# Optimization experiments

Hardware: AMD Instinct MI355X
Metric: run time of the kernel (lower is better)

The kernel has to match this reference:

```python
import jax, jax.numpy as jnp
import numpy as np

EPS = 1e-13

def masked_softmax(scores, mask):
    # scores: [B, L1, L2], mask: [B, L2] binary float
    # ESIM-style: softmax(scores * mask) * mask, renormalized.
    m = mask[:, None, :]                      # [B, 1, L2]
    r = jax.nn.softmax(scores * m, axis=-1) * m
    return r / (r.sum(axis=-1, keepdims=True) + EPS)

def weighted_sum(attn, tensor, mask):
    # attn: [B, L1, L2], tensor: [B, L2, D], mask: [B, L1]
    return jnp.matmul(attn, tensor) * mask[:, :, None]

def setup_inputs() -> dict:
    key = jax.random.key(0)
    k1, k2, k3, k4 = jax.random.split(key, 4)
    B, Lp, Lh, D = 64, 512, 512, 600
    encoded_premise = jax.random.normal(k1, (B, Lp, D), dtype=jnp.float32)
    encoded_hypothesis = jax.random.normal(k2, (B, Lh, D), dtype=jnp.float32)
    # binary padding masks (1 = valid token)
    premise_mask = (jax.random.uniform(k3, (B, Lp)) > 0.15).astype(jnp.float32)
    hypothesis_mask = (jax.random.uniform(k4, (B, Lh)) > 0.15).astype(jnp.float32)
    return {"encoded_premise": encoded_premise, "premise_mask": premise_mask,
            "encoded_hypothesis": encoded_hypothesis, "hypothesis_mask": hypothesis_mask}

def reference(encoded_premise, premise_mask, encoded_hypothesis, hypothesis_mask):
    # shared cross-attention score matrix [B, Lp, Lh]
    attn = jnp.einsum('bpd,bhd->bph', encoded_premise, encoded_hypothesis)
    a_p = masked_softmax(attn, hypothesis_mask)                    # [B, Lp, Lh]
    a_h = masked_softmax(attn.transpose(0, 2, 1), premise_mask)    # [B, Lh, Lp]
    weighted_premise = weighted_sum(a_p, encoded_hypothesis, premise_mask)      # [B, Lp, D]
    weighted_hypothesis = weighted_sum(a_h, encoded_premise, hypothesis_mask)   # [B, Lh, D]
    return (weighted_premise, weighted_hypothesis)
```

## Files before the change

kernel.cpp:

```cpp
#include <hip/hip_runtime.h>
#include <hip/hip_bf16.h>

#define DEVB 64
#define LSEQ 512
#define DDIM 600

typedef short short8 __attribute__((ext_vector_type(8)));
typedef float f32x4 __attribute__((ext_vector_type(4)));
typedef _Float16 f16x8 __attribute__((ext_vector_type(8)));
typedef _Float16 f16x4 __attribute__((ext_vector_type(4)));

constexpr int LDP = 40;

__device__ __forceinline__ unsigned short f2bf(float x) {
    union { float f; unsigned u; } v; v.f = x;
    unsigned r = v.u + 0x7fffu + ((v.u >> 16) & 1u);
    return (unsigned short)(r >> 16);
}
__device__ __forceinline__ f32x4 mfma16(short8 a, short8 b, f32x4 c) {
    return __builtin_amdgcn_mfma_f32_16x16x32_bf16(a, b, c, 0, 0, 0);
}
__device__ __forceinline__ f32x4 mfma16h(f16x8 a, f16x8 b, f32x4 c) {
    return __builtin_amdgcn_mfma_f32_16x16x32_f16(a, b, c, 0, 0, 0);
}

__global__ __launch_bounds__(256) void prep_both(
    const float* __restrict__ P, const float* __restrict__ H,
    _Float16* __restrict__ Phi, _Float16* __restrict__ Plo,
    _Float16* __restrict__ Hhi,
    _Float16* __restrict__ pT, _Float16* __restrict__ hT)
{
    int blk = blockIdx.x;
    const float* X; _Float16 *Xhi, *Xlo, *XT;
    if (blk < DEVB * 80) { X = P; Xhi = Phi; Xlo = Plo; XT = pT; }
    else { blk -= DEVB * 80; X = H; Xhi = Hhi; Xlo = nullptr; XT = hT; }

    int b   = blk / 80;
    int rem = blk % 80;
    int r0  = (rem / 10) << 6;
    int d0  = (rem % 10) << 6;
    const float* Xb = X + (size_t)b * LSEQ * DDIM;
    _Float16* Hib = Xhi + (size_t)b * LSEQ * DDIM;
    _Float16* Lob = Xlo ? (Xlo + (size_t)b * LSEQ * DDIM) : nullptr;

    __shared__ _Float16 T[64 * 66];
    int t = threadIdx.x;
#pragma unroll
    for (int it = 0; it < 2; ++it) {
        int g  = t + (it << 8);
        int ri = g >> 3;
        int dc = (g & 7) << 3;
        if (d0 + dc < DDIM) {
            const float* src = Xb + (size_t)(r0 + ri) * DDIM + d0 + dc;
            float4 x0 = *(const float4*)src;
            float4 x1 = *(const float4*)(src + 4);
            f16x8 hi, lo;
            hi[0] = (_Float16)x0.x; lo[0] = (_Float16)(x0.x - (float)hi[0]);
            hi[1] = (_Float16)x0.y; lo[1] = (_Float16)(x0.y - (float)hi[1]);
            hi[2] = (_Float16)x0.z; lo[2] = (_Float16)(x0.z - (float)hi[2]);
            hi[3] = (_Float16)x0.w; lo[3] = (_Float16)(x0.w - (float)hi[3]);
            hi[4] = (_Float16)x1.x; lo[4] = (_Float16)(x1.x - (float)hi[4]);
            hi[5] = (_Float16)x1.y; lo[5] = (_Float16)(x1.y - (float)hi[5]);
            hi[6] = (_Float16)x1.z; lo[6] = (_Float16)(x1.z - (float)hi[6]);
            hi[7] = (_Float16)x1.w; lo[7] = (_Float16)(x1.w - (float)hi[7]);
            *(f16x8*)(Hib + (size_t)(r0 + ri) * DDIM + d0 + dc) = hi;
            if (Lob) *(f16x8*)(Lob + (size_t)(r0 + ri) * DDIM + d0 + dc) = lo;
#pragma unroll
            for (int j = 0; j < 8; ++j)
                T[(dc + j) * 66 + ri] = hi[j];
        }
    }
    if (XT) {
        __syncthreads();
        int d  = t >> 2;
        int ch = (t & 3) << 4;
        if (d0 + d < DDIM) {
            unsigned buf[8];
#pragma unroll
            for (int i = 0; i < 8; ++i)
                buf[i] = *(const unsigned*)&T[d * 66 + ch + 2 * i];
            unsigned* dst = (unsigned*)(XT + ((size_t)b * DDIM + d0 + d) * LSEQ + r0 + ch);
            *(uint4*)(dst)     = *(uint4*)&buf[0];
            *(uint4*)(dst + 4) = *(uint4*)&buf[4];
        }
    }
}

__global__ __launch_bounds__(256) void attn_gemm(
    const _Float16* __restrict__ Phi, const _Float16* __restrict__ Plo,
    const _Float16* __restrict__ Hhi, float* __restrict__ attn)
{
    const int bid = blockIdx.x;
    const int swz = (bid & 7) * 128 + (bid >> 3);
    const int b  = swz >> 4;
    const int pt = ((swz >> 2) & 3) << 7;
    const int ht = (swz & 3) << 7;
    const _Float16* Pbh = Phi + ((size_t)b * LSEQ + pt) * DDIM;
    const _Float16* Pbl = Plo + ((size_t)b * LSEQ + pt) * DDIM;
    const _Float16* Hb  = Hhi + ((size_t)b * LSEQ + ht) * DDIM;
    float* Ab = attn + (size_t)b * LSEQ * LSEQ;

    __shared__ _Float16 Ah[2][128 * 32], Al[2][128 * 32], Bh[2][128 * 32];

    const int t    = threadIdx.x;
    const int lane = t & 63;
    const int wave = t >> 6;
    const int wm = (wave >> 1) << 6;
    const int wn = (wave & 1) << 6;
    const int fr = lane & 15;
    const int fq = lane >> 4;
    const int srow = t >> 2;
    const int sc8  = (t & 3) << 3;

    const int wchunk = (t & 3) ^ ((srow >> 1) & 3);
    const int woff   = srow * 32 + (wchunk << 3);
    const int rcoff  = ((fq ^ ((fr >> 1) & 3)) << 3);

    f16x8 pf[6];
    const f16x8 zz = {0, 0, 0, 0, 0, 0, 0, 0};
    auto issue = [&](int k0) {
        bool ok = (k0 + sc8) < DDIM;
#pragma unroll
        for (int r = 0; r < 2; ++r) {
            size_t off = (size_t)(srow + (r << 6)) * DDIM + k0 + sc8;
            pf[r * 3 + 0] = ok ? *(const f16x8*)(Pbh + off) : zz;
            pf[r * 3 + 1] = ok ? *(const f16x8*)(Pbl + off) : zz;
            pf[r * 3 + 2] = ok ? *(const f16x8*)(Hb  + off) : zz;
        }
    };
    auto wr = [&](int buf) {
#pragma unroll
        for (int r = 0; r < 2; ++r) {
            int off = woff + (r << 11);
            *(f16x8*)&Ah[buf][off] = pf[r * 3 + 0];
            *(f16x8*)&Al[buf][off] = pf[r * 3 + 1];
            *(f16x8*)&Bh[buf][off] = pf[r * 3 + 2];
        }
    };

    issue(0);
    wr(0);
    issue(32);
    __syncthreads();

    f32x4 acc[4][4];
#pragma unroll
    for (int i = 0; i < 4; ++i)
#pragma unroll
        for (int j = 0; j < 4; ++j) acc[i][j] = (f32x4){0.f, 0.f, 0.f, 0.f};

    constexpr int NK = 19;
    int cur = 0;
    for (int it = 0; it < NK; ++it) {
        f16x8 ah[4], al[4], bh[4];
#pragma unroll
        for (int i = 0; i < 4; ++i) {
            int ra = (wm + (i << 4) + fr) * 32 + rcoff;
            int rb = (wn + (i << 4) + fr) * 32 + rcoff;
            ah[i] = *(const f16x8*)&Ah[cur][ra];
            al[i] = *(const f16x8*)&Al[cur][ra];
            bh[i] = *(const f16x8*)&Bh[cur][rb];
        }
        if (it + 1 < NK) {
            wr(cur ^ 1);
            if (it + 2 < NK) issue((it + 2) << 5);
        }
#pragma unroll
        for (int mi = 0; mi < 4; ++mi)
#pragma unroll
            for (int ni = 0; ni < 4; ++ni) {
                f32x4 c = acc[mi][ni];
                c = mfma16h(ah[mi], bh[ni], c);
                c = mfma16h(al[mi], bh[ni], c);
                acc[mi][ni] = c;
            }
        __syncthreads();
        cur ^= 1;
    }

#pragma unroll
    for (int mi = 0; mi < 4; ++mi)
#pragma unroll
        for (int ni = 0; ni < 4; ++ni)
#pragma unroll
            for (int j = 0; j < 4; ++j) {
                int p = pt + wm + (mi << 4) + (fq << 2) + j;
                int h = ht + wn + (ni << 4) + fr;
                Ab[(size_t)p * LSEQ + h] = acc[mi][ni][j];
            }
}

__global__ __launch_bounds__(256) void stats_w1(
    const float* __restrict__ attn, const float* __restrict__ hmask,
    const float* __restrict__ pmask,
    float* __restrict__ M1, float* __restrict__ R1,
    _Float16* __restrict__ W1,
    float* __restrict__ Mp, float* __restrict__ Tp, float* __restrict__ Sp)
{
    int b      = blockIdx.x >> 3;
    int stripe = blockIdx.x & 7;
    int lane   = threadIdx.x & 63;
    int wave   = threadIdx.x >> 6;
    const float* hm = hmask + (b << 9);
    const float* pm = pmask + (b << 9);

    float4 m0 = *(const float4*)(hm + (lane << 3));
    float4 m1 = *(const float4*)(hm + (lane << 3) + 4);
    float mk[8] = {m0.x, m0.y, m0.z, m0.w, m1.x, m1.y, m1.z, m1.w};

    float cM[8], cT[8], cS[8];
#pragma unroll
    for (int j = 0; j < 8; ++j) { cM[j] = -1e30f; cT[j] = 0.f; cS[j] = 0.f; }

    for (int i = 0; i < 16; ++i) {
        int row   = (stripe << 6) + (wave << 4) + i;
        int rowid = (b << 9) + row;
        const float* rp = attn + (size_t)rowid * LSEQ + (lane << 3);
        float4 s0 = *(const float4*)rp;
        float4 s1 = *(const float4*)(rp + 4);
        float s[8] = {s0.x, s0.y, s0.z, s0.w, s1.x, s1.y, s1.z, s1.w};

        float v[8];
#pragma unroll
        for (int j = 0; j < 8; ++j) v[j] = s[j] * mk[j];
        float mx = -1e30f;
#pragma unroll
        for (int j = 0; j < 8; ++j) mx = fmaxf(mx, v[j]);
#pragma unroll
        for (int off = 32; off; off >>= 1) mx = fmaxf(mx, __shfl_xor(mx, off));

        float e[8], T = 0.f, S = 0.f;
#pragma unroll
        for (int j = 0; j < 8; ++j) { e[j] = __expf(v[j] - mx); T += mk[j] * e[j]; S += e[j]; }
#pragma unroll
        for (int off = 32; off; off >>= 1) { T += __shfl_xor(T, off); S += __shfl_xor(S, off); }
        float R = 1.f / (T + 1e-13f * S);

        if (W1) {
            union { f16x8 v8; _Float16 h[8]; } wv;
#pragma unroll
            for (int j = 0; j < 8; ++j) wv.h[j] = (_Float16)(mk[j] * e[j] * R);
            *(f16x8*)(W1 + (size_t)rowid * LSEQ + (lane << 3)) = wv.v8;
        }
        if (lane == 0) { M1[rowid] = mx; R1[rowid] = R; }

        float pmv = pm[row];
#pragma unroll
        for (int j = 0; j < 8; ++j) {
            float v2 = s[j] * pmv;
            float nm = fmaxf(cM[j], v2);
            float sc = __expf(cM[j] - nm);
            float e2 = __expf(v2 - nm);
            cT[j] = cT[j] * sc + pmv * e2;
            cS[j] = cS[j] * sc + e2;
            cM[j] = nm;
        }
    }

    __shared__ float LM[4][512], LT[4][512], LS[4][512];
#pragma unroll
    for (int j = 0; j < 8; ++j) {
        int c = (lane << 3) + j;
        LM[wave][c] = cM[j]; LT[wave][c] = cT[j]; LS[wave][c] = cS[j];
    }
    __syncthreads();

    size_t base = (size_t)((b << 3) + stripe) * 512;
    for (int cc = threadIdx.x; cc < 512; cc += 256) {
        float gm = fmaxf(fmaxf(LM[0][cc], LM[1][cc]), fmaxf(LM[2][cc], LM[3][cc]));
        float gT = 0.f, gS = 0.f;
#pragma unroll
        for (int w = 0; w < 4; ++w) {
            float sc = __expf(LM[w][cc] - gm);
            gT += LT[w][cc] * sc;
            gS += LS[w][cc] * sc;
        }
        Mp[base + cc] = gm; Tp[base + cc] = gT; Sp[base + cc] = gS;
    }
}

__global__ __launch_bounds__(256) void col_merge(
    const float* __restrict__ Mp, const float* __restrict__ Tp,
    const float* __restrict__ Sp, float* __restrict__ M2, float* __restrict__ R2)
{
    int b = blockIdx.x >> 1;
    int c = ((blockIdx.x & 1) << 8) + threadIdx.x;
    float gm = -1e30f, gT = 0.f, gS = 0.f;
#pragma unroll
    for (int st = 0; st < 8; ++st) {
        size_t idx = (size_t)((b << 3) + st) * 512 + c;
        float m = Mp[idx], tt = Tp[idx], ss = Sp[idx];
        float nm  = fmaxf(gm, m);
        float sc1 = __expf(gm - nm), sc2 = __expf(m - nm);
        gT = gT * sc1 + tt * sc2;
        gS = gS * sc1 + ss * sc2;
        gm = nm;
    }
    M2[(b << 9) + c] = gm;
    R2[(b << 9) + c] = 1.f / (gT + 1e-13f * gS);
}

__global__ __launch_bounds__(256) void w2gen_m(
    const float* __restrict__ attn, const float* __restrict__ pmask,
    const float* __restrict__ Mp, const float* __restrict__ Tp,
    const float* __restrict__ Sp, _Float16* __restrict__ W2)
{
    int blk = blockIdx.x;
    int b  = blk >> 5;
    int p0 = ((blk >> 2) & 7) << 6;
    int h0 = (blk & 3) << 7;
    const float* Ab = attn + (size_t)b * LSEQ * LSEQ;
    const float* pm = pmask + (b << 9);

    __shared__ float sM[128], sR[128];
    __shared__ _Float16 T[128 * 66];
    int t = threadIdx.x;
    if (t < 128) {
        float gm = -1e30f, gT = 0.f, gS = 0.f;
#pragma unroll
        for (int st = 0; st < 8; ++st) {
            size_t idx = (size_t)((b << 3) + st) * 512 + h0 + t;
            float m = Mp[idx], tt = Tp[idx], ss = Sp[idx];
            float nm  = fmaxf(gm, m);
            float sc1 = __expf(gm - nm), sc2 = __expf(m - nm);
            gT = gT * sc1 + tt * sc2;
            gS = gS * sc1 + ss * sc2;
            gm = nm;
        }
        sM[t] = gm;
        sR[t] = 1.f / (gT + 1e-13f * gS);
    }
    __syncthreads();

#pragma unroll
    for (int it = 0; it < 8; ++it) {
        int g  = t + (it << 8);
        int pi = g >> 5;
        int hc = (g & 31) << 2;
        float4 x = *(const float4*)(Ab + (size_t)(p0 + pi) * LSEQ + h0 + hc);
        float pv = pm[p0 + pi];
        _Float16 w0 = 0, w1 = 0, w2 = 0, w3 = 0;
        if (pv != 0.f) {
            w0 = (_Float16)(__expf(x.x - sM[hc + 0]) * sR[hc + 0]);
            w1 = (_Float16)(__expf(x.y - sM[hc + 1]) * sR[hc + 1]);
            w2 = (_Float16)(__expf(x.z - sM[hc + 2]) * sR[hc + 2]);
            w3 = (_Float16)(__expf(x.w - sM[hc + 3]) * sR[hc + 3]);
        }
        T[(hc + 0) * 66 + pi] = w0;
        T[(hc + 1) * 66 + pi] = w1;
        T[(hc + 2) * 66 + pi] = w2;
        T[(hc + 3) * 66 + pi] = w3;
    }
    __syncthreads();

    int h  = t >> 1;
    int po = (t & 1) << 5;
    unsigned buf[16];
#pragma unroll
    for (int i = 0; i < 16; ++i)
        buf[i] = *(const unsigned*)&T[h * 66 + po + 2 * i];
    unsigned* dst = (unsigned*)(W2 + ((size_t)(b << 9) + h0 + h) * LSEQ + p0 + po);
#pragma unroll
    for (int i = 0; i < 4; ++i)
        *(uint4*)(dst + 4 * i) = *(uint4*)&buf[4 * i];
}

__global__ __launch_bounds__(256) void gemm_fp16(
    const _Float16* __restrict__ W, const _Float16* __restrict__ BT,
    const float* __restrict__ mask_m, float* __restrict__ out)
{
    const int bid = blockIdx.x;
    const int swz = (bid & 7) * 160 + (bid >> 3);
    const int b   = swz / 20;
    const int rem = swz % 20;
    const int m0  = (rem / 5) << 7;
    const int n0  = (rem % 5) << 7;
    const _Float16* Wb = W  + (size_t)b * LSEQ * LSEQ;
    const _Float16* Bb = BT + (size_t)b * DDIM * LSEQ;

    __shared__ _Float16 Wl[2][128 * 32];
    __shared__ _Float16 Bl[2][128 * 32];

    const int t    = threadIdx.x;
    const int lane = t & 63;
    const int wave = t >> 6;
    const int wm = (wave >> 1) << 6;
    const int wn = (wave & 1) << 6;
    const int fr = lane & 15;
    const int fq = lane >> 4;
    const int srow = t >> 2;
    const int sc8  = (t & 3) << 3;

    const int wchunk = (t & 3) ^ ((srow >> 1) & 3);
    const int woff   = srow * 32 + (wchunk << 3);
    const int rcoff  = ((fq ^ ((fr >> 1) & 3)) << 3);

    f16x8 pw[2], pb[2];
    const f16x8 zz = {0, 0, 0, 0, 0, 0, 0, 0};
    auto issue = [&](int k0) {
#pragma unroll
        for (int r = 0; r < 2; ++r) {
            int row = srow + (r << 6);
            pw[r] = *(const f16x8*)(Wb + (size_t)(m0 + row) * LSEQ + k0 + sc8);
            int nrow = n0 + row;
            pb[r] = (nrow < DDIM) ? *(const f16x8*)(Bb + (size_t)nrow * LSEQ + k0 + sc8) : zz;
        }
    };
    auto wr = [&](int buf) {
#pragma unroll
        for (int r = 0; r < 2; ++r) {
            int off = woff + (r << 11);
            *(f16x8*)&Wl[buf][off] = pw[r];
            *(f16x8*)&Bl[buf][off] = pb[r];
        }
    };

    issue(0);
    wr(0);
    issue(32);
    __syncthreads();

    f32x4 acc[4][4];
#pragma unroll
    for (int i = 0; i < 4; ++i)
#pragma unroll
        for (int j = 0; j < 4; ++j) acc[i][j] = (f32x4){0.f, 0.f, 0.f, 0.f};

    constexpr int NK = 16;
    int cur = 0;
    for (int it = 0; it < NK; ++it) {
        f16x8 af[4], bfr[4];
#pragma unroll
        for (int i = 0; i < 4; ++i) {
            af[i]  = *(const f16x8*)&Wl[cur][(wm + (i << 4) + fr) * 32 + rcoff];
            bfr[i] = *(const f16x8*)&Bl[cur][(wn + (i << 4) + fr) * 32 + rcoff];
        }
        if (it + 1 < NK) {
            wr(cur ^ 1);
            if (it + 2 < NK) issue((it + 2) << 5);
        }
#pragma unroll
        for (int mi = 0; mi < 4; ++mi)
#pragma unroll
            for (int ni = 0; ni < 4; ++ni)
                acc[mi][ni] = mfma16h(af[mi], bfr[ni], acc[mi][ni]);
        __syncthreads();
        cur ^= 1;
    }

    const float* mmb = mask_m + (b << 9) + m0;
#pragma unroll
    for (int mi = 0; mi < 4; ++mi)
#pragma unroll
        for (int j = 0; j < 4; ++j) {
            int row = wm + (mi << 4) + (fq << 2) + j;
            float mm = mmb[row];
#pragma unroll
            for (int ni = 0; ni < 4; ++ni) {
                int d = n0 + wn + (ni << 4) + fr;
                if (d < DDIM)
                    out[((size_t)(b << 9) + m0 + row) * DDIM + d] = mm * acc[mi][ni][j];
            }
        }
}

template <int TRANSA>
__global__ __launch_bounds__(256) void wsum(
    const float* __restrict__ attn, const float* __restrict__ Bsrc,
    const float* __restrict__ mask_k, const float* __restrict__ mask_m,
    const float* __restrict__ Mst, const float* __restrict__ Rst,
    float* __restrict__ out)
{
    const int blk = blockIdx.x;
    const int b   = blk / 20;
    const int rem = blk % 20;
    const int m0  = (rem / 5) << 7;
    const int n0  = (rem % 5) << 7;

    const float* Ab  = attn + (size_t)b * LSEQ * LSEQ;
    const float* Bb  = Bsrc + (size_t)b * LSEQ * DDIM;
    const float* mkb = mask_k + (b << 9);

    __shared__ unsigned short Wl[128 * LDP];
    __shared__ unsigned short Bl[128 * LDP];
    __shared__ float Ml[128], Rl[128], Mm[128];

    const int t    = threadIdx.x;
    const int lane = t & 63;
    const int wave = t >> 6;
    const int wm = (wave >> 1) << 6;
    const int wn = (wave & 1) << 6;
    const int fr = lane & 15;
    const int fq = lane >> 4;

    if (t < 128) {
        Ml[t] = Mst[(b << 9) + m0 + t];
        Rl[t] = Rst[(b << 9) + m0 + t];
        Mm[t] = mask_m[(b << 9) + m0 + t];
    }
    __syncthreads();

    f32x4 acc[4][4];
#pragma unroll
    for (int i = 0; i < 4; ++i)
#pragma unroll
        for (int j = 0; j < 4; ++j) acc[i][j] = (f32x4){0.f, 0.f, 0.f, 0.f};

    for (int k0 = 0; k0 < LSEQ; k0 += 32) {
        if constexpr (TRANSA == 0) {
#pragma unroll
            for (int r = 0; r < 4; ++r) {
                int idx = t + (r << 8);
                int row = idx >> 3;
                int c4  = (idx & 7) << 2;
                float4 x  = *(const float4*)(Ab + (size_t)(m0 + row) * LSEQ + k0 + c4);
                float4 km = *(const float4*)(mkb + k0 + c4);
                float Mv = Ml[row], Rv = Rl[row];
                ushort4 w;
                w.x = (km.x != 0.f) ? f2bf(__expf(x.x - Mv) * Rv) : (unsigned short)0;
                w.y = (km.y != 0.f) ? f2bf(__expf(x.y - Mv) * Rv) : (unsigned short)0;
                w.z = (km.z != 0.f) ? f2bf(__expf(x.z - Mv) * Rv) : (unsigned short)0;
                w.w = (km.w != 0.f) ? f2bf(__expf(x.w - Mv) * Rv) : (unsigned short)0;
                *(ushort4*)&Wl[row * LDP + c4] = w;
            }
        } else {
#pragma unroll
            for (int r = 0; r < 4; ++r) {
                int mh = t & 127;
                int pq = (t >> 7) + (r << 1);
                float Mv = Ml[mh], Rv = Rl[mh];
                ushort4 w;
#pragma unroll
                for (int j = 0; j < 4; ++j) {
                    int k = k0 + (pq << 2) + j;
                    float x  = Ab[(size_t)k * LSEQ + m0 + mh];
                    float km = mkb[k];
                    ((unsigned short*)&w)[j] =
                        (km != 0.f) ? f2bf(__expf(x - Mv) * Rv) : (unsigned short)0;
                }
                *(ushort4*)&Wl[mh * LDP + (pq << 2)] = w;
            }
        }
#pragma unroll
        for (int r = 0; r < 4; ++r) {
            int d  = t & 127;
            int kq = (t >> 7) + (r << 1);
            bool valid = (n0 + d) < DDIM;
            ushort4 v;
#pragma unroll
            for (int j = 0; j < 4; ++j) {
                int k = k0 + (kq << 2) + j;
                float x = valid ? Bb[(size_t)k * DDIM + n0 + d] : 0.f;
                ((unsigned short*)&v)[j] = f2bf(x);
            }
            *(ushort4*)&Bl[d * LDP + (kq << 2)] = v;
        }
        __syncthreads();

        short8 af[4], bfr[4];
#pragma unroll
        for (int i = 0; i < 4; ++i) {
            af[i]  = *(const short8*)&Wl[(wm + (i << 4) + fr) * LDP + (fq << 3)];
            bfr[i] = *(const short8*)&Bl[(wn + (i << 4) + fr) * LDP + (fq << 3)];
        }
#pragma unroll
        for (int mi = 0; mi < 4; ++mi)
#pragma unroll
            for (int ni = 0; ni < 4; ++ni)
                acc[mi][ni] = mfma16(af[mi], bfr[ni], acc[mi][ni]);
        __syncthreads();
    }

#pragma unroll
    for (int mi = 0; mi < 4; ++mi)
#pragma unroll
        for (int j = 0; j < 4; ++j) {
            int row = wm + (mi << 4) + (fq << 2) + j;
            float mm = Mm[row];
#pragma unroll
            for (int ni = 0; ni < 4; ++ni) {
                int d = n0 + wn + (ni << 4) + fr;
                if (d < DDIM)
                    out[((size_t)(b << 9) + m0 + row) * DDIM + d] = mm * acc[mi][ni][j];
            }
        }
}

extern "C" void kernel_launch(void* const* d_in, const int* in_sizes, int n_in,
                              void* d_out, int out_size, void* d_ws, size_t ws_size,
                              hipStream_t stream)
{
    const float* P  = (const float*)d_in[0];
    const float* pm = (const float*)d_in[1];
    const float* H  = (const float*)d_in[2];
    const float* hm = (const float*)d_in[3];
    float* out = (float*)d_out;
    char* o  = (char*)d_out;
    char* ws = (char*)d_ws;

    const size_t E = (size_t)DEVB * LSEQ * DDIM;

    _Float16* Phi = (_Float16*)o;
    _Float16* Plo = Phi + E;
    _Float16* Hhi = Plo + E;
    _Float16* hT  = Hhi + E;
    _Float16* W1  = Hhi;

    const size_t fast_need = 143654912;

    if (ws_size >= fast_need) {
        float*     attn = (float*)ws;
        _Float16*  pT   = (_Float16*)(ws + 67108864);
        _Float16*  W2   = (_Float16*)(ws + 67108864 + 39321600);
        float*     Mp   = (float*)(ws + 139984896);
        float*     Tp   = Mp + (size_t)DEVB * 8 * 512;
        float*     Sp   = Tp + (size_t)DEVB * 8 * 512;
        float*     M1   = Sp + (size_t)DEVB * 8 * 512;
        float*     R1   = M1 + DEVB * LSEQ;

        prep_both<<<DEVB * 160, 256, 0, stream>>>(P, H, Phi, Plo, Hhi, pT, hT);
        attn_gemm<<<DEVB * 16, 256, 0, stream>>>(Phi, Plo, Hhi, attn);
        stats_w1<<<DEVB * 8, 256, 0, stream>>>(attn, hm, pm, M1, R1, W1, Mp, Tp, Sp);
        w2gen_m<<<DEVB * 32, 256, 0, stream>>>(attn, pm, Mp, Tp, Sp, W2);
        gemm_fp16<<<DEVB * 20, 256, 0, stream>>>(W1, hT, pm, out);
        gemm_fp16<<<DEVB * 20, 256, 0, stream>>>(W2, pT, hm, out + E);
    } else {
        float* attn = (float*)ws;
        float* Mp   = (float*)(ws + 67108864);
        float* Tp   = Mp + (size_t)DEVB * 8 * 512;
        float* Sp   = Tp + (size_t)DEVB * 8 * 512;
        float* M1   = Sp + (size_t)DEVB * 8 * 512;
        float* R1   = M1 + DEVB * LSEQ;
        float* M2   = R1 + DEVB * LSEQ;
        float* R2   = M2 + DEVB * LSEQ;

        prep_both<<<DEVB * 160, 256, 0, stream>>>(P, H, Phi, Plo, Hhi, nullptr, nullptr);
        attn_gemm<<<DEVB * 16, 256, 0, stream>>>(Phi, Plo, Hhi, attn);
        stats_w1<<<DEVB * 8, 256, 0, stream>>>(attn, hm, pm, M1, R1, nullptr, Mp, Tp, Sp);
        col_merge<<<DEVB * 2, 256, 0, stream>>>(Mp, Tp, Sp, M2, R2);
        wsum<0><<<DEVB * 20, 256, 0, stream>>>(attn, H, hm, pm, M1, R1, out);
        wsum<1><<<DEVB * 20, 256, 0, stream>>>(attn, P, pm, hm, M2, R2, out + E);
    }
}
```

Baseline: 340.5 us.

## Fuse fp16 hi/lo split into attention GEMM loads, drop staged copies

```diff
diff --git a/kernel.cpp b/kernel.cpp
--- a/kernel.cpp
+++ b/kernel.cpp
@@ -24,24 +24,20 @@
     return __builtin_amdgcn_mfma_f32_16x16x32_f16(a, b, c, 0, 0, 0);
 }
 
-__global__ __launch_bounds__(256) void prep_both(
+__global__ __launch_bounds__(256) void transcvt2(
     const float* __restrict__ P, const float* __restrict__ H,
-    _Float16* __restrict__ Phi, _Float16* __restrict__ Plo,
-    _Float16* __restrict__ Hhi,
     _Float16* __restrict__ pT, _Float16* __restrict__ hT)
 {
     int blk = blockIdx.x;
-    const float* X; _Float16 *Xhi, *Xlo, *XT;
-    if (blk < DEVB * 80) { X = P; Xhi = Phi; Xlo = Plo; XT = pT; }
-    else { blk -= DEVB * 80; X = H; Xhi = Hhi; Xlo = nullptr; XT = hT; }
+    const float* X; _Float16* XT;
+    if (blk < DEVB * 80) { X = P; XT = pT; }
+    else { blk -= DEVB * 80; X = H; XT = hT; }
 
     int b   = blk / 80;
     int rem = blk % 80;
     int r0  = (rem / 10) << 6;
     int d0  = (rem % 10) << 6;
     const float* Xb = X + (size_t)b * LSEQ * DDIM;
-    _Float16* Hib = Xhi + (size_t)b * LSEQ * DDIM;
-    _Float16* Lob = Xlo ? (Xlo + (size_t)b * LSEQ * DDIM) : nullptr;
 
     __shared__ _Float16 T[64 * 66];
     int t = threadIdx.x;
@@ -54,50 +50,38 @@
             const float* src = Xb + (size_t)(r0 + ri) * DDIM + d0 + dc;
             float4 x0 = *(const float4*)src;
             float4 x1 = *(const float4*)(src + 4);
-            f16x8 hi, lo;
-            hi[0] = (_Float16)x0.x; lo[0] = (_Float16)(x0.x - (float)hi[0]);
-            hi[1] = (_Float16)x0.y; lo[1] = (_Float16)(x0.y - (float)hi[1]);
-            hi[2] = (_Float16)x0.z; lo[2] = (_Float16)(x0.z - (float)hi[2]);
-            hi[3] = (_Float16)x0.w; lo[3] = (_Float16)(x0.w - (float)hi[3]);
-            hi[4] = (_Float16)x1.x; lo[4] = (_Float16)(x1.x - (float)hi[4]);
-            hi[5] = (_Float16)x1.y; lo[5] = (_Float16)(x1.y - (float)hi[5]);
-            hi[6] = (_Float16)x1.z; lo[6] = (_Float16)(x1.z - (float)hi[6]);
-            hi[7] = (_Float16)x1.w; lo[7] = (_Float16)(x1.w - (float)hi[7]);
-            *(f16x8*)(Hib + (size_t)(r0 + ri) * DDIM + d0 + dc) = hi;
-            if (Lob) *(f16x8*)(Lob + (size_t)(r0 + ri) * DDIM + d0 + dc) = lo;
+            float xf[8] = {x0.x, x0.y, x0.z, x0.w, x1.x, x1.y, x1.z, x1.w};
 #pragma unroll
             for (int j = 0; j < 8; ++j)
-                T[(dc + j) * 66 + ri] = hi[j];
-        }
-    }
-    if (XT) {
-        __syncthreads();
-        int d  = t >> 2;
-        int ch = (t & 3) << 4;
-        if (d0 + d < DDIM) {
-            unsigned buf[8];
-#pragma unroll
-            for (int i = 0; i < 8; ++i)
-                buf[i] = *(const unsigned*)&T[d * 66 + ch + 2 * i];
-            unsigned* dst = (unsigned*)(XT + ((size_t)b * DDIM + d0 + d) * LSEQ + r0 + ch);
-            *(uint4*)(dst)     = *(uint4*)&buf[0];
-            *(uint4*)(dst + 4) = *(uint4*)&buf[4];
-        }
+                T[(dc + j) * 66 + ri] = (_Float16)xf[j];
+        }
+    }
+    __syncthreads();
+
+    int d  = t >> 2;
+    int ch = (t & 3) << 4;
+    if (d0 + d < DDIM) {
+        unsigned buf[8];
+#pragma unroll
+        for (int i = 0; i < 8; ++i)
+            buf[i] = *(const unsigned*)&T[d * 66 + ch + 2 * i];
+        unsigned* dst = (unsigned*)(XT + ((size_t)b * DDIM + d0 + d) * LSEQ + r0 + ch);
+        *(uint4*)(dst)     = *(uint4*)&buf[0];
+        *(uint4*)(dst + 4) = *(uint4*)&buf[4];
     }
 }
 
 __global__ __launch_bounds__(256) void attn_gemm(
-    const _Float16* __restrict__ Phi, const _Float16* __restrict__ Plo,
-    const _Float16* __restrict__ Hhi, float* __restrict__ attn)
+    const float* __restrict__ P, const float* __restrict__ H,
+    float* __restrict__ attn)
 {
     const int bid = blockIdx.x;
     const int swz = (bid & 7) * 128 + (bid >> 3);
     const int b  = swz >> 4;
     const int pt = ((swz >> 2) & 3) << 7;
     const int ht = (swz & 3) << 7;
-    const _Float16* Pbh = Phi + ((size_t)b * LSEQ + pt) * DDIM;
-    const _Float16* Pbl = Plo + ((size_t)b * LSEQ + pt) * DDIM;
-    const _Float16* Hb  = Hhi + ((size_t)b * LSEQ + ht) * DDIM;
+    const float* Pb = P + ((size_t)b * LSEQ + pt) * DDIM;
+    const float* Hb = H + ((size_t)b * LSEQ + ht) * DDIM;
     float* Ab = attn + (size_t)b * LSEQ * LSEQ;
 
     __shared__ _Float16 Ah[2][128 * 32], Al[2][128 * 32], Bh[2][128 * 32];
@@ -116,25 +100,42 @@
     const int woff   = srow * 32 + (wchunk << 3);
     const int rcoff  = ((fq ^ ((fr >> 1) & 3)) << 3);
 
-    f16x8 pf[6];
-    const f16x8 zz = {0, 0, 0, 0, 0, 0, 0, 0};
+    float4 pf[8];
+    const float4 fz = {0.f, 0.f, 0.f, 0.f};
     auto issue = [&](int k0) {
         bool ok = (k0 + sc8) < DDIM;
 #pragma unroll
         for (int r = 0; r < 2; ++r) {
-            size_t off = (size_t)(srow + (r << 6)) * DDIM + k0 + sc8;
-            pf[r * 3 + 0] = ok ? *(const f16x8*)(Pbh + off) : zz;
-            pf[r * 3 + 1] = ok ? *(const f16x8*)(Pbl + off) : zz;
-            pf[r * 3 + 2] = ok ? *(const f16x8*)(Hb  + off) : zz;
+            size_t base = (size_t)(srow + (r << 6)) * DDIM + k0 + sc8;
+            if (ok) {
+                pf[r * 4 + 0] = *(const float4*)(Pb + base);
+                pf[r * 4 + 1] = *(const float4*)(Pb + base + 4);
+                pf[r * 4 + 2] = *(const float4*)(Hb + base);
+                pf[r * 4 + 3] = *(const float4*)(Hb + base + 4);
+            } else {
+                pf[r * 4 + 0] = fz; pf[r * 4 + 1] = fz;
+                pf[r * 4 + 2] = fz; pf[r * 4 + 3] = fz;
+            }
         }
     };
     auto wr = [&](int buf) {
 #pragma unroll
         for (int r = 0; r < 2; ++r) {
+            float4 a0 = pf[r * 4 + 0], a1 = pf[r * 4 + 1];
+            float4 h0 = pf[r * 4 + 2], h1 = pf[r * 4 + 3];
+            float af[8] = {a0.x, a0.y, a0.z, a0.w, a1.x, a1.y, a1.z, a1.w};
+            float hf[8] = {h0.x, h0.y, h0.z, h0.w, h1.x, h1.y, h1.z, h1.w};
+            f16x8 hi, lo, bh;
+#pragma unroll
+            for (int j = 0; j < 8; ++j) {
+                hi[j] = (_Float16)af[j];
+                lo[j] = (_Float16)(af[j] - (float)hi[j]);
+                bh[j] = (_Float16)hf[j];
+            }
             int off = woff + (r << 11);
-            *(f16x8*)&Ah[buf][off] = pf[r * 3 + 0];
-            *(f16x8*)&Al[buf][off] = pf[r * 3 + 1];
-            *(f16x8*)&Bh[buf][off] = pf[r * 3 + 2];
+            *(f16x8*)&Ah[buf][off] = hi;
+            *(f16x8*)&Al[buf][off] = lo;
+            *(f16x8*)&Bh[buf][off] = bh;
         }
     };
 
@@ -600,11 +601,8 @@
 
     const size_t E = (size_t)DEVB * LSEQ * DDIM;
 
-    _Float16* Phi = (_Float16*)o;
-    _Float16* Plo = Phi + E;
-    _Float16* Hhi = Plo + E;
-    _Float16* hT  = Hhi + E;
-    _Float16* W1  = Hhi;
+    _Float16* hT = (_Float16*)(o + 78643200);
+    _Float16* W1 = (_Float16*)(o + 117964800);
 
     const size_t fast_need = 143654912;
 
@@ -618,8 +616,8 @@
         float*     M1   = Sp + (size_t)DEVB * 8 * 512;
         float*     R1   = M1 + DEVB * LSEQ;
 
-        prep_both<<<DEVB * 160, 256, 0, stream>>>(P, H, Phi, Plo, Hhi, pT, hT);
-        attn_gemm<<<DEVB * 16, 256, 0, stream>>>(Phi, Plo, Hhi, attn);
+        transcvt2<<<DEVB * 160, 256, 0, stream>>>(P, H, pT, hT);
+        attn_gemm<<<DEVB * 16, 256, 0, stream>>>(P, H, attn);
         stats_w1<<<DEVB * 8, 256, 0, stream>>>(attn, hm, pm, M1, R1, W1, Mp, Tp, Sp);
         w2gen_m<<<DEVB * 32, 256, 0, stream>>>(attn, pm, Mp, Tp, Sp, W2);
         gemm_fp16<<<DEVB * 20, 256, 0, stream>>>(W1, hT, pm, out);
@@ -634,8 +632,7 @@
         float* M2   = R1 + DEVB * LSEQ;
         float* R2   = M2 + DEVB * LSEQ;
 
-        prep_both<<<DEVB * 160, 256, 0, stream>>>(P, H, Phi, Plo, Hhi, nullptr, nullptr);
-        attn_gemm<<<DEVB * 16, 256, 0, stream>>>(Phi, Plo, Hhi, attn);
+        attn_gemm<<<DEVB * 16, 256, 0, stream>>>(P, H, attn);
         stats_w1<<<DEVB * 8, 256, 0, stream>>>(attn, hm, pm, M1, R1, nullptr, Mp, Tp, Sp);
         col_merge<<<DEVB * 2, 256, 0, stream>>>(Mp, Tp, Sp, M2, R2);
         wsum<0><<<DEVB * 20, 256, 0, stream>>>(attn, H, hm, pm, M1, R1, out);
```

Result: faster. 318.1 us (-6.6%).
